# Performance work log

Hardware: AMD Instinct MI355X
Metric: run time of the kernel (lower is better)

The kernel has to match this reference:

```python
import jax, jax.numpy as jnp
import numpy as np

L, B, S, D, H = 3, 64, 512, 1024, 512  # layers, batch, seq, input(=2H), hidden


def setup_inputs() -> dict:
    key = jax.random.key(0)
    ks = jax.random.split(key, 13)
    s = lambda k, shape: jax.random.normal(k, shape, jnp.float32) * 0.02
    return {
        "x": jax.random.normal(ks[0], (B, S, D), jnp.float32),
        "fw_W": s(ks[1], (L, D + H, 3 * H)),
        "fw_b": s(ks[2], (L, 3 * H)),
        "bw_W": s(ks[3], (L, D + H, 3 * H)),
        "bw_b": s(ks[4], (L, 3 * H)),
        "h0f": s(ks[5], (L, H)),
        "c0f": s(ks[6], (L, H)),
        "h0b": s(ks[7], (L, H)),
        "c0b": s(ks[8], (L, H)),
        "proj_W": s(ks[9], (L, 2 * H, 2 * H)),
        "proj_b": s(ks[10], (L, 2 * H)),
        "in_proj_W": s(ks[11], (D, 2 * H)),
        "in_proj_b": s(ks[12], (2 * H,)),
    }


def _lstm_dir(x_tbd, W, b, h0, c0):
    """Run the coupled 3-gate cell over time. x_tbd: [S,B,D]. Returns [S,B,H]."""
    bsz = x_tbd.shape[1]

    def step(carry, xt):
        h, c = carry
        g = jnp.concatenate([xt, h], axis=-1) @ W + b  # [B, 3H]
        i, j, o = jnp.split(g, 3, axis=-1)
        i = jax.nn.sigmoid(i)
        c = (1.0 - i) * c + i * jnp.tanh(j)
        h = jnp.tanh(c) * jax.nn.sigmoid(o)
        return (h, c), h

    init = (jnp.broadcast_to(h0, (bsz, H)), jnp.broadcast_to(c0, (bsz, H)))
    _, hs = jax.lax.scan(step, init, x_tbd)
    return hs


def reference(x, fw_W, fw_b, bw_W, bw_b, h0f, c0f, h0b, c0b, proj_W, proj_b, in_proj_W, in_proj_b):
    inputs = x  # [B,S,D]
    for l in range(L):
        xt = jnp.transpose(inputs, (1, 0, 2))  # [S,B,D]
        hf = _lstm_dir(xt, fw_W[l], fw_b[l], h0f[l], c0f[l])            # [S,B,H]
        hb = _lstm_dir(xt[::-1], bw_W[l], bw_b[l], h0b[l], c0b[l])[::-1]  # [S,B,H]
        out = jnp.transpose(jnp.concatenate([hf, hb], axis=-1), (1, 0, 2))  # [B,S,2H]
        gate = jax.nn.sigmoid(out @ proj_W[l] + proj_b[l])
        if l == 0:
            inputs = x @ in_proj_W + in_proj_b  # project raw input to 2H for highway
        inputs = gate * out + (1.0 - gate) * inputs
    return inputs
```

## Files before the change

### kernel.cpp

```cpp
#include <hip/hip_runtime.h>
#include <stdint.h>

typedef short bf16x8 __attribute__((ext_vector_type(8)));
typedef short s16x4 __attribute__((ext_vector_type(4)));
typedef float f32x4 __attribute__((ext_vector_type(4)));
typedef unsigned int u32;
typedef unsigned short u16;
typedef unsigned long long u64;

#define OFF_WXT  0ull
#define OFF_WHF  18874368ull
#define OFF_CTR  28311552ull
#define OFF_PRJT 37748736ull
#define OFF_IPJT 44040192ull
#define OFF_XB   46137344ull
#define OFF_G    113246208ull
#define OFF_OCAT 314572800ull
#define OFF_INP  381681664ull
#define OFF_HB   515899392ull
#define WS_NEED  516161536ull

__device__ __forceinline__ float b2f(u32 u){ return __uint_as_float(u<<16); }
__device__ __forceinline__ u16 f2b(float f){
  u32 i = __float_as_uint(f);
  return (u16)((i + 0x7FFFu + ((i>>16)&1u))>>16);
}
__device__ __forceinline__ float sigm(float x){ return 1.f/(1.f+__expf(-x)); }
__device__ __forceinline__ float tanh_f(float x){
  x = fminf(fmaxf(x,-15.f),15.f);
  float e = __expf(2.f*x);
  return (e-1.f)/(e+1.f);
}
__device__ __forceinline__ void gl_lds16(const void* g, void* l){
  __builtin_amdgcn_global_load_lds((const __attribute__((address_space(1))) u32*)g,
                                   (__attribute__((address_space(3))) u32*)l, 16, 0, 0);
}

__global__ void k_convx(const float4* __restrict__ x, u64* __restrict__ xb){
  long i = (long)blockIdx.x*blockDim.x + threadIdx.x;
  float4 v = x[i];
  xb[i] = (u64)f2b(v.x) | ((u64)f2b(v.y)<<16) | ((u64)f2b(v.z)<<32) | ((u64)f2b(v.w)<<48);
}

__global__ __launch_bounds__(256)
void k_tr(const float* __restrict__ fw, const float* __restrict__ bw,
          const float* __restrict__ pw, const float* __restrict__ ipw,
          u16* __restrict__ wxt, u16* __restrict__ pjt, u16* __restrict__ ipjt){
  __shared__ u16 lds[64][66];
  const int b = blockIdx.x;
  const float* src; u16* dst; int srcLD, dstLD, r0, c0;
  if (b < 2304){
    int mat = b / 384, tt = b % 384;
    int kt = tt % 16, nt = tt / 16;
    int d = mat / 3, l = mat % 3;
    src = (d ? bw : fw) + (size_t)l*1536*1536; srcLD = 1536;
    dst = wxt + (size_t)mat*1536*1024;        dstLD = 1024;
    r0 = kt*64; c0 = nt*64;
  } else if (b < 3072){
    int bb = b - 2304, mat = bb / 256, tt = bb % 256;
    int kt = tt % 16, nt = tt / 16;
    src = pw + (size_t)mat*1048576; srcLD = 1024;
    dst = pjt + (size_t)mat*1048576; dstLD = 1024;
    r0 = kt*64; c0 = nt*64;
  } else {
    int tt = b - 3072;
    int kt = tt % 16, nt = tt / 16;
    src = ipw; srcLD = 1024; dst = ipjt; dstLD = 1024;
    r0 = kt*64; c0 = nt*64;
  }
  const int tr = threadIdx.x >> 6, tc = threadIdx.x & 63;
  #pragma unroll
  for (int i=0;i<16;i++){
    int r = i*4 + tr;
    lds[r][tc] = f2b(src[(size_t)(r0+r)*srcLD + c0 + tc]);
  }
  __syncthreads();
  #pragma unroll
  for (int i=0;i<16;i++){
    int nr = i*4 + tr;
    dst[(size_t)(c0+nr)*dstLD + r0 + tc] = lds[tc][nr];
  }
}

__global__ __launch_bounds__(256)
void k_whf2(const float* __restrict__ fw, const float* __restrict__ bw, u16* __restrict__ out){
  __shared__ u16 lds[64][66];
  const int b = blockIdx.x;
  const int mat = b / 192, tt = b % 192;
  const int rt = tt & 7, ct = tt >> 3;
  const int l = mat >> 1, d = mat & 1;
  const float* W = (d ? bw : fw) + (size_t)l*1536*1536;
  const int tr = threadIdx.x >> 6, tc = threadIdx.x & 63;
  #pragma unroll
  for (int i=0;i<16;i++){
    int r = i*4 + tr;
    lds[r][tc] = f2b(W[(size_t)(1024 + rt*64 + r)*1536 + ct*64 + tc]);
  }
  __syncthreads();
  const int t = threadIdx.x;
  const int lane = t >> 2;
  const int e0 = (t & 3)*2;
  u32* o32 = (u32*)out;
  #pragma unroll
  for (int kkl=0; kkl<2; ++kkl){
    int rl = kkl*32 + (lane>>4)*8 + e0;
    int kk = rt*2 + kkl;
    #pragma unroll
    for (int cg=0; cg<4; ++cg){
      int col = ct*64 + cg*16;
      int g = col >> 9;
      int wg = (col & 511) >> 4;
      size_t base16 = (size_t)l*1572864 + (size_t)((d*32+wg)*3 + g)*8192 + (size_t)kk*512;
      u16 lo = lds[rl    ][cg*16 + (lane&15)];
      u16 hi = lds[rl + 1][cg*16 + (lane&15)];
      o32[base16/2 + t] = (u32)lo | ((u32)hi<<16);
    }
  }
}

template<int V>
__global__ __launch_bounds__(256)
void gemm_bt(const u16* __restrict__ A, const u16* __restrict__ Bt,
             const float* __restrict__ bias, int K,
             u16* __restrict__ Gout, int dir,
             float* __restrict__ inputs,
             const u16* __restrict__ ocat, u16* __restrict__ xbout,
             float* __restrict__ dout)
{
  __shared__ u16 As[128*64];
  __shared__ u16 Bs[128*64];
  const int tid = threadIdx.x, wid = tid>>6, lane = tid&63;
  const int wr = wid>>1, wc = wid&1;
  const int mblk = blockIdx.x & 255;
  const int nblk = blockIdx.x >> 8;
  f32x4 acc[4][4];
  #pragma unroll
  for (int i=0;i<4;i++)
    #pragma unroll
    for (int j=0;j<4;j++) acc[i][j] = (f32x4){0.f,0.f,0.f,0.f};
  const size_t Kb = (size_t)K*2;
  const char* Ab = (const char*)A + (size_t)(mblk*128)*Kb;
  const char* Bb = (const char*)Bt + (size_t)(nblk*128)*Kb;
  const int r8 = lane>>3, c8 = lane&7;
  for (int kt=0; kt<K/64; ++kt){
    __syncthreads();
    #pragma unroll
    for (int i=0;i<4;i++){
      const int instr = wid*4 + i;
      const int row = instr*8 + r8;
      const int so = (c8*16) ^ ((row&7)<<4);
      gl_lds16(Ab + (size_t)row*Kb + kt*128 + so, (char*)As + instr*1024);
      gl_lds16(Bb + (size_t)row*Kb + kt*128 + so, (char*)Bs + instr*1024);
    }
    __syncthreads();
    #pragma unroll
    for (int ks=0; ks<2; ++ks){
      bf16x8 af[4], bfv[4];
      #pragma unroll
      for (int mt=0;mt<4;mt++){
        int r = wr*64 + mt*16 + (lane&15);
        int kb = (ks*64 + ((lane>>4)*16)) ^ ((r&7)<<4);
        af[mt] = *(const bf16x8*)((const char*)As + r*128 + kb);
      }
      #pragma unroll
      for (int nt=0;nt<4;nt++){
        int r = wc*64 + nt*16 + (lane&15);
        int kb = (ks*64 + ((lane>>4)*16)) ^ ((r&7)<<4);
        bfv[nt] = *(const bf16x8*)((const char*)Bs + r*128 + kb);
      }
      #pragma unroll
      for (int mt=0;mt<4;mt++)
        #pragma unroll
        for (int nt=0;nt<4;nt++)
          acc[mt][nt] = __builtin_amdgcn_mfma_f32_16x16x32_bf16(af[mt], bfv[nt], acc[mt][nt], 0,0,0);
    }
  }
  const int mb = mblk*128 + wr*64;
  const int nb = nblk*128 + wc*64;
  #pragma unroll
  for (int nt=0;nt<4;nt++){
    const int n = nb + nt*16 + (lane&15);
    const float bv = bias[n];
    #pragma unroll
    for (int mt=0;mt<4;mt++){
      #pragma unroll
      for (int r=0;r<4;r++){
        const int m = mb + mt*16 + (lane>>4)*4 + r;
        float v = acc[mt][nt][r] + bv;
        if (V==0){
          int b = m >> 9, t = m & 511;
          int tp = dir ? (511 - t) : t;
          int brow = b & 15;
          size_t idx = (((size_t)tp*96 + (n>>9)*32 + ((n&511)>>4))*4 + (b>>4))*256
                     + ((brow>>2)<<6) + ((n&15)<<2) + (brow&3);
          Gout[idx] = f2b(v);
        } else if (V==1){
          inputs[(size_t)m*1024 + n] = v;
        } else {
          float g = sigm(v);
          size_t a = (size_t)m*1024 + n;
          float o = b2f((u32)ocat[a]);
          float nv = g*o + (1.f-g)*inputs[a];
          if (dout) dout[a] = nv;
          else { inputs[a] = nv; xbout[a] = f2b(nv); }
        }
      }
    }
  }
}

__global__ __launch_bounds__(512, 1)
void lstm_rec(const u16* __restrict__ Whf, const u16* __restrict__ G,
              u16* __restrict__ hb,
              const float* __restrict__ h0f_, const float* __restrict__ c0f_,
              const float* __restrict__ h0b_, const float* __restrict__ c0b_,
              u16* __restrict__ ocat, u32* __restrict__ ctr, int lay)
{
  const int blk = blockIdx.x;
  const int d  = blk >> 6;
  const int bi = (blk >> 4) & 3;
  const int ci = blk & 15;
  const int tid = threadIdx.x;
  const int wave = tid >> 6, lane = tid & 63;

  __shared__ u16 hlds[16*544];
  __shared__ float ldsg[3][16][37];
  __shared__ float ldsc[16][37];

  const int g = wave >> 1, half = wave & 1;
  const bool isg = (wave < 6);

  bf16x8 w[16];
  if (isg){
    const int wgg = ci*2 + half;
    const u16* wb = Whf + (((size_t)(d*32+wgg)*3 + g)*1024 + (size_t)lane)*8;
    #pragma unroll
    for (int kk=0;kk<16;kk++) w[kk] = *(const bf16x8*)(wb + kk*512);
  }
  const float* h0 = d ? h0b_ : h0f_;
  const float* c0 = d ? c0b_ : c0f_;
  u16* hbd = hb + (size_t)d*65536;
  const u16* Gd = G + (size_t)d*50331648ull;
  u32* av = ctr + (size_t)(d*4+bi)*512;
  const u32 labase = (u32)lay * 513u;

  if (tid < 256){
    int b = tid >> 4, c2 = (tid & 15)*2;
    int col = ci*32 + c2;
    u32 pk = (u32)f2b(h0[col]) | ((u32)f2b(h0[col+1])<<16);
    __hip_atomic_store((u32*)(hbd + (size_t)(bi*16+b)*512 + col), pk,
                       __ATOMIC_RELAXED, __HIP_MEMORY_SCOPE_AGENT);
    ldsc[b][c2]   = c0[col];
    ldsc[b][c2+1] = c0[col+1];
  }
  __syncthreads();
  if (tid==0)
    __hip_atomic_store(av + ci*32, labase + 1u, __ATOMIC_RELAXED, __HIP_MEMORY_SCOPE_AGENT);

  const int ntile = g*32 + ci*2 + half;
  s16x4 q{};
  if (isg)
    q = *(const s16x4*)(Gd + (((size_t)0*96 + ntile)*4 + bi)*256 + lane*4);

  const int srow = lane >> 2;
  const int part = lane & 3;
  const int p0 = wave*2, p1 = wave*2 + 1;
  const int swzw = (srow & 7) << 4;
  char* hlrow = (char*)hlds + srow*1088;
  const int mr = lane & 15;
  const char* ab = (const char*)hlds + mr*1088;
  const int c16 = (lane>>4)*16;
  const int swzr = (mr & 7) << 4;

  for (int t=0; t<512; ++t){
    const u32 tgt = labase + (u32)t + 1u;
    const u64* hsrc = (const u64*)(hbd + (size_t)(t&1)*32768) + (size_t)bi*2048;
    while (__hip_atomic_load(av + p0*32, __ATOMIC_RELAXED, __HIP_MEMORY_SCOPE_AGENT) < tgt) {}
    while (__hip_atomic_load(av + p1*32, __ATOMIC_RELAXED, __HIP_MEMORY_SCOPE_AGENT) < tgt) {}
    asm volatile("" ::: "memory");
    u64 a0 = __hip_atomic_load(hsrc + srow*128 + p0*8 + part*2,     __ATOMIC_RELAXED, __HIP_MEMORY_SCOPE_AGENT);
    u64 a1 = __hip_atomic_load(hsrc + srow*128 + p0*8 + part*2 + 1, __ATOMIC_RELAXED, __HIP_MEMORY_SCOPE_AGENT);
    u64 b0 = __hip_atomic_load(hsrc + srow*128 + p1*8 + part*2,     __ATOMIC_RELAXED, __HIP_MEMORY_SCOPE_AGENT);
    u64 b1 = __hip_atomic_load(hsrc + srow*128 + p1*8 + part*2 + 1, __ATOMIC_RELAXED, __HIP_MEMORY_SCOPE_AGENT);
    *(u64*)(hlrow + ((p0*64 + part*16) ^ swzw))     = a0;
    *(u64*)(hlrow + ((p0*64 + part*16) ^ swzw) + 8) = a1;
    *(u64*)(hlrow + ((p1*64 + part*16) ^ swzw))     = b0;
    *(u64*)(hlrow + ((p1*64 + part*16) ^ swzw) + 8) = b1;
    __syncthreads();

    if (isg){
      f32x4 ea={0.f,0.f,0.f,0.f}, eb={0.f,0.f,0.f,0.f};
      #pragma unroll
      for (int kk=0;kk<16;kk+=2){
        bf16x8 a0v = *(const bf16x8*)(ab + ((kk*64     + c16) ^ swzr));
        bf16x8 a1v = *(const bf16x8*)(ab + ((kk*64+64  + c16) ^ swzr));
        ea = __builtin_amdgcn_mfma_f32_16x16x32_bf16(a0v, w[kk],   ea, 0,0,0);
        eb = __builtin_amdgcn_mfma_f32_16x16x32_bf16(a1v, w[kk+1], eb, 0,0,0);
      }
      const int bb = (lane>>4)*4;
      const int cc = half*16 + (lane&15);
      #pragma unroll
      for (int r=0;r<4;r++)
        ldsg[g][bb+r][cc] = ea[r] + eb[r] + b2f((u32)(u16)q[r]);
    }
    __syncthreads();

    const int t_o = d ? (511 - t) : t;
    u16* hnxt = hbd + (size_t)((t+1)&1)*32768;
    if (tid < 256){
      int b = tid>>4, c2 = (tid&15)*2;
      float i0 = sigm(ldsg[0][b][c2]);
      float i1 = sigm(ldsg[0][b][c2+1]);
      float cn0 = (1.f-i0)*ldsc[b][c2]   + i0*tanh_f(ldsg[1][b][c2]);
      float cn1 = (1.f-i1)*ldsc[b][c2+1] + i1*tanh_f(ldsg[1][b][c2+1]);
      ldsc[b][c2] = cn0; ldsc[b][c2+1] = cn1;
      float hv0 = tanh_f(cn0)*sigm(ldsg[2][b][c2]);
      float hv1 = tanh_f(cn1)*sigm(ldsg[2][b][c2+1]);
      u32 pk = (u32)f2b(hv0) | ((u32)f2b(hv1)<<16);
      int gb = bi*16 + b, col = ci*32 + c2;
      __hip_atomic_store((u32*)(hnxt + (size_t)gb*512 + col), pk,
                         __ATOMIC_RELAXED, __HIP_MEMORY_SCOPE_AGENT);
      *(u32*)(ocat + (((size_t)(gb*512 + t_o))<<10) + (d<<9) + col) = pk;
    }
    __syncthreads();

    if (tid==0)
      __hip_atomic_store(av + ci*32, labase + (u32)t + 2u,
                         __ATOMIC_RELAXED, __HIP_MEMORY_SCOPE_AGENT);
    if (isg){
      int tn = (t+1 < 512) ? (t+1) : 511;
      q = *(const s16x4*)(Gd + (((size_t)tn*96 + ntile)*4 + bi)*256 + lane*4);
    }
  }
}

extern "C" void kernel_launch(void* const* d_in, const int* in_sizes, int n_in,
                              void* d_out, int out_size, void* d_ws, size_t ws_size,
                              hipStream_t stream)
{
  (void)in_sizes; (void)n_in; (void)out_size;
  if (ws_size < WS_NEED) return;
  const float* x      = (const float*)d_in[0];
  const float* fw_W   = (const float*)d_in[1];
  const float* fw_b   = (const float*)d_in[2];
  const float* bw_W   = (const float*)d_in[3];
  const float* bw_b   = (const float*)d_in[4];
  const float* h0f    = (const float*)d_in[5];
  const float* c0f    = (const float*)d_in[6];
  const float* h0b    = (const float*)d_in[7];
  const float* c0b    = (const float*)d_in[8];
  const float* proj_W = (const float*)d_in[9];
  const float* proj_b = (const float*)d_in[10];
  const float* ipW    = (const float*)d_in[11];
  const float* ipb    = (const float*)d_in[12];
  char* ws = (char*)d_ws;
  u16* WXT  = (u16*)(ws + OFF_WXT);
  u16* WHF  = (u16*)(ws + OFF_WHF);
  u16* PRJT = (u16*)(ws + OFF_PRJT);
  u16* IPJT = (u16*)(ws + OFF_IPJT);
  u16* XB   = (u16*)(ws + OFF_XB);
  u16* GB   = (u16*)(ws + OFF_G);
  u16* OCAT = (u16*)(ws + OFF_OCAT);
  float* INP= (float*)(ws + OFF_INP);
  u16* HB   = (u16*)(ws + OFF_HB);
  u32* CTR  = (u32*)(ws + OFF_CTR);

  hipMemsetAsync(CTR, 0, 16384, stream);
  k_convx<<<32768, 256, 0, stream>>>((const float4*)x, (u64*)XB);
  k_tr<<<3328, 256, 0, stream>>>(fw_W, bw_W, proj_W, ipW, WXT, PRJT, IPJT);
  k_whf2<<<1152, 256, 0, stream>>>(fw_W, bw_W, WHF);

  gemm_bt<1><<<2048, 256, 0, stream>>>(XB, IPJT, ipb, 1024, nullptr, 0, INP, nullptr, nullptr, nullptr);

  for (int l=0; l<3; ++l){
    gemm_bt<0><<<3072, 256, 0, stream>>>(XB, WXT + (size_t)l*1572864, fw_b + l*1536, 1024,
                                         GB, 0, nullptr, nullptr, nullptr, nullptr);
    gemm_bt<0><<<3072, 256, 0, stream>>>(XB, WXT + (size_t)(3+l)*1572864, bw_b + l*1536, 1024,
                                         GB + 50331648ull, 1, nullptr, nullptr, nullptr, nullptr);
    {
      const u16* whfl = WHF + (size_t)l*1572864;
      const u16* gbp  = GB;
      u16* hbp = HB;
      const float* p1 = h0f + l*512;
      const float* p2 = c0f + l*512;
      const float* p3 = h0b + l*512;
      const float* p4 = c0b + l*512;
      u16* ocp = OCAT;
      u32* ctp = CTR;
      int lay = l;
      void* args[] = { (void*)&whfl, (void*)&gbp, (void*)&hbp,
                       (void*)&p1, (void*)&p2, (void*)&p3, (void*)&p4,
                       (void*)&ocp, (void*)&ctp, (void*)&lay };
      hipLaunchCooperativeKernel((void*)lstm_rec, dim3(128), dim3(512), args, 0, stream);
    }
    gemm_bt<2><<<2048, 256, 0, stream>>>(OCAT, PRJT + (size_t)l*1048576, proj_b + l*1024, 1024,
                                         nullptr, 0, INP, OCAT, XB,
                                         (l==2) ? (float*)d_out : nullptr);
  }
}
```

Before: 6.287 ms.

## Shrink recurrent LSTM grid to 32 blocks with all three gates per wave

Restructures the recurrent kernel so each block covers 128 hidden columns, and each wave holds the i, j and o gate weights in registers and computes all three gates for its 16 columns. The cell update then runs in registers, with no LDS round trip and one fewer barrier per step. The hidden-state output write to ocat is deferred to the next step and read from the LDS copy. This cuts the number of blocks that must synchronise across the GPU each timestep (128 to 32) and the spin-wait fanout. In exchange each block does more MFMA work per step and carries much higher register pressure from holding 48 weight vectors per lane.

```diff
diff --git a/kernel.cpp b/kernel.cpp
--- a/kernel.cpp
+++ b/kernel.cpp
@@ -209,7 +209,7 @@
   }
 }
 
-__global__ __launch_bounds__(512, 1)
+__global__ __launch_bounds__(512, 2)
 void lstm_rec(const u16* __restrict__ Whf, const u16* __restrict__ G,
               u16* __restrict__ hb,
               const float* __restrict__ h0f_, const float* __restrict__ c0f_,
@@ -217,25 +217,26 @@
               u16* __restrict__ ocat, u32* __restrict__ ctr, int lay)
 {
   const int blk = blockIdx.x;
-  const int d  = blk >> 6;
-  const int bi = (blk >> 4) & 3;
-  const int ci = blk & 15;
+  const int d  = blk >> 4;
+  const int bi = (blk >> 2) & 3;
+  const int ci = blk & 3;
   const int tid = threadIdx.x;
   const int wave = tid >> 6, lane = tid & 63;
 
   __shared__ u16 hlds[16*544];
-  __shared__ float ldsg[3][16][37];
-  __shared__ float ldsc[16][37];
-
-  const int g = wave >> 1, half = wave & 1;
-  const bool isg = (wave < 6);
-
-  bf16x8 w[16];
-  if (isg){
-    const int wgg = ci*2 + half;
-    const u16* wb = Whf + (((size_t)(d*32+wgg)*3 + g)*1024 + (size_t)lane)*8;
-    #pragma unroll
-    for (int kk=0;kk<16;kk++) w[kk] = *(const bf16x8*)(wb + kk*512);
+
+  const int nt   = ci*8 + wave;
+  const int wcol = nt*16 + (lane&15);
+
+  bf16x8 w0[16], w1[16], w2[16];
+  {
+    const u16* W = Whf + ((size_t)(d*32+nt)*3)*8192 + (size_t)lane*8;
+    #pragma unroll
+    for (int kk=0;kk<16;kk++) w0[kk] = *(const bf16x8*)(W + kk*512);
+    #pragma unroll
+    for (int kk=0;kk<16;kk++) w1[kk] = *(const bf16x8*)(W + 8192 + kk*512);
+    #pragma unroll
+    for (int kk=0;kk<16;kk++) w2[kk] = *(const bf16x8*)(W + 16384 + kk*512);
   }
   const float* h0 = d ? h0b_ : h0f_;
   const float* c0 = d ? c0b_ : c0f_;
@@ -244,92 +245,102 @@
   u32* av = ctr + (size_t)(d*4+bi)*512;
   const u32 labase = (u32)lay * 513u;
 
-  if (tid < 256){
-    int b = tid >> 4, c2 = (tid & 15)*2;
-    int col = ci*32 + c2;
+  float c[4];
+  { float cv = c0[wcol]; c[0]=cv; c[1]=cv; c[2]=cv; c[3]=cv; }
+
+  #pragma unroll
+  for (int it=0; it<2; ++it){
+    int p = tid + it*512;
+    int row = bi*16 + (p>>6);
+    int col = ci*128 + (p&63)*2;
     u32 pk = (u32)f2b(h0[col]) | ((u32)f2b(h0[col+1])<<16);
-    __hip_atomic_store((u32*)(hbd + (size_t)(bi*16+b)*512 + col), pk,
+    __hip_atomic_store((u32*)(hbd + (size_t)row*512 + col), pk,
                        __ATOMIC_RELAXED, __HIP_MEMORY_SCOPE_AGENT);
-    ldsc[b][c2]   = c0[col];
-    ldsc[b][c2+1] = c0[col+1];
   }
   __syncthreads();
   if (tid==0)
     __hip_atomic_store(av + ci*32, labase + 1u, __ATOMIC_RELAXED, __HIP_MEMORY_SCOPE_AGENT);
 
-  const int ntile = g*32 + ci*2 + half;
-  s16x4 q{};
-  if (isg)
-    q = *(const s16x4*)(Gd + (((size_t)0*96 + ntile)*4 + bi)*256 + lane*4);
-
+  s16x4 qi{}, qj{}, qo{};
+  {
+    const u16* Gt = Gd + ((size_t)nt*4 + bi)*256 + lane*4;
+    qi = *(const s16x4*)(Gt);
+    qj = *(const s16x4*)(Gt + 32768);
+    qo = *(const s16x4*)(Gt + 65536);
+  }
+
+  const int sp   = wave >> 1;
+  const int scb  = sp*128 + (wave&1)*64;
   const int srow = lane >> 2;
-  const int part = lane & 3;
-  const int p0 = wave*2, p1 = wave*2 + 1;
-  const int swzw = (srow & 7) << 4;
-  char* hlrow = (char*)hlds + srow*1088;
+  const int scol = scb + (lane&3)*16;
+  const size_t gbase = ((size_t)(bi*16+srow))*128 + (size_t)(scol>>2);
+  const int sx0  = scol*2;
+  const int swzw = (srow&7)<<4;
+  char* lrow = (char*)hlds + srow*1088;
+
   const int mr = lane & 15;
   const char* ab = (const char*)hlds + mr*1088;
   const int c16 = (lane>>4)*16;
-  const int swzr = (mr & 7) << 4;
-
-  for (int t=0; t<512; ++t){
+  const int swzr = (mr&7)<<4;
+
+  for (int t=0; t<=512; ++t){
     const u32 tgt = labase + (u32)t + 1u;
-    const u64* hsrc = (const u64*)(hbd + (size_t)(t&1)*32768) + (size_t)bi*2048;
-    while (__hip_atomic_load(av + p0*32, __ATOMIC_RELAXED, __HIP_MEMORY_SCOPE_AGENT) < tgt) {}
-    while (__hip_atomic_load(av + p1*32, __ATOMIC_RELAXED, __HIP_MEMORY_SCOPE_AGENT) < tgt) {}
+    while (__hip_atomic_load(av + sp*32, __ATOMIC_RELAXED, __HIP_MEMORY_SCOPE_AGENT) < tgt) {}
     asm volatile("" ::: "memory");
-    u64 a0 = __hip_atomic_load(hsrc + srow*128 + p0*8 + part*2,     __ATOMIC_RELAXED, __HIP_MEMORY_SCOPE_AGENT);
-    u64 a1 = __hip_atomic_load(hsrc + srow*128 + p0*8 + part*2 + 1, __ATOMIC_RELAXED, __HIP_MEMORY_SCOPE_AGENT);
-    u64 b0 = __hip_atomic_load(hsrc + srow*128 + p1*8 + part*2,     __ATOMIC_RELAXED, __HIP_MEMORY_SCOPE_AGENT);
-    u64 b1 = __hip_atomic_load(hsrc + srow*128 + p1*8 + part*2 + 1, __ATOMIC_RELAXED, __HIP_MEMORY_SCOPE_AGENT);
-    *(u64*)(hlrow + ((p0*64 + part*16) ^ swzw))     = a0;
-    *(u64*)(hlrow + ((p0*64 + part*16) ^ swzw) + 8) = a1;
-    *(u64*)(hlrow + ((p1*64 + part*16) ^ swzw))     = b0;
-    *(u64*)(hlrow + ((p1*64 + part*16) ^ swzw) + 8) = b1;
+    const u64* hsrc = (const u64*)(hbd + (size_t)(t&1)*32768);
+    u64 v0 = __hip_atomic_load(hsrc + gbase,     __ATOMIC_RELAXED, __HIP_MEMORY_SCOPE_AGENT);
+    u64 v1 = __hip_atomic_load(hsrc + gbase + 1, __ATOMIC_RELAXED, __HIP_MEMORY_SCOPE_AGENT);
+    u64 v2 = __hip_atomic_load(hsrc + gbase + 2, __ATOMIC_RELAXED, __HIP_MEMORY_SCOPE_AGENT);
+    u64 v3 = __hip_atomic_load(hsrc + gbase + 3, __ATOMIC_RELAXED, __HIP_MEMORY_SCOPE_AGENT);
+    *(u64*)(lrow + ( sx0       ^ swzw))      = v0;
+    *(u64*)(lrow + ( sx0       ^ swzw) + 8)  = v1;
+    *(u64*)(lrow + ((sx0 + 16) ^ swzw))      = v2;
+    *(u64*)(lrow + ((sx0 + 16) ^ swzw) + 8)  = v3;
     __syncthreads();
 
-    if (isg){
-      f32x4 ea={0.f,0.f,0.f,0.f}, eb={0.f,0.f,0.f,0.f};
-      #pragma unroll
-      for (int kk=0;kk<16;kk+=2){
-        bf16x8 a0v = *(const bf16x8*)(ab + ((kk*64     + c16) ^ swzr));
-        bf16x8 a1v = *(const bf16x8*)(ab + ((kk*64+64  + c16) ^ swzr));
-        ea = __builtin_amdgcn_mfma_f32_16x16x32_bf16(a0v, w[kk],   ea, 0,0,0);
-        eb = __builtin_amdgcn_mfma_f32_16x16x32_bf16(a1v, w[kk+1], eb, 0,0,0);
-      }
-      const int bb = (lane>>4)*4;
-      const int cc = half*16 + (lane&15);
-      #pragma unroll
-      for (int r=0;r<4;r++)
-        ldsg[g][bb+r][cc] = ea[r] + eb[r] + b2f((u32)(u16)q[r]);
-    }
-    __syncthreads();
-
-    const int t_o = d ? (511 - t) : t;
+    if (t > 0){
+      int lr = ci*4 + (tid>>7);
+      int col4 = (tid&127)*4;
+      u64 hv = *(const u64*)((const char*)hlds + lr*1088 + ((col4*2) ^ ((lr&7)<<4)));
+      int t_o = d ? (512 - t) : (t - 1);
+      *(u64*)(ocat + (size_t)((bi*16+lr)*512 + t_o)*1024 + (d<<9) + col4) = hv;
+    }
+    if (t == 512) break;
+
+    f32x4 ai={0.f,0.f,0.f,0.f}, aj={0.f,0.f,0.f,0.f}, ao={0.f,0.f,0.f,0.f};
+    #pragma unroll
+    for (int kk=0;kk<16;kk++){
+      bf16x8 a = *(const bf16x8*)(ab + ((kk*64 + c16) ^ swzr));
+      ai = __builtin_amdgcn_mfma_f32_16x16x32_bf16(a, w0[kk], ai, 0,0,0);
+      aj = __builtin_amdgcn_mfma_f32_16x16x32_bf16(a, w1[kk], aj, 0,0,0);
+      ao = __builtin_amdgcn_mfma_f32_16x16x32_bf16(a, w2[kk], ao, 0,0,0);
+    }
+
     u16* hnxt = hbd + (size_t)((t+1)&1)*32768;
-    if (tid < 256){
-      int b = tid>>4, c2 = (tid&15)*2;
-      float i0 = sigm(ldsg[0][b][c2]);
-      float i1 = sigm(ldsg[0][b][c2+1]);
-      float cn0 = (1.f-i0)*ldsc[b][c2]   + i0*tanh_f(ldsg[1][b][c2]);
-      float cn1 = (1.f-i1)*ldsc[b][c2+1] + i1*tanh_f(ldsg[1][b][c2+1]);
-      ldsc[b][c2] = cn0; ldsc[b][c2+1] = cn1;
-      float hv0 = tanh_f(cn0)*sigm(ldsg[2][b][c2]);
-      float hv1 = tanh_f(cn1)*sigm(ldsg[2][b][c2+1]);
-      u32 pk = (u32)f2b(hv0) | ((u32)f2b(hv1)<<16);
-      int gb = bi*16 + b, col = ci*32 + c2;
-      __hip_atomic_store((u32*)(hnxt + (size_t)gb*512 + col), pk,
+    #pragma unroll
+    for (int r=0;r<4;r++){
+      float gi = sigm(ai[r] + b2f((u32)(u16)qi[r]));
+      float gj = tanh_f(aj[r] + b2f((u32)(u16)qj[r]));
+      float go = sigm(ao[r] + b2f((u32)(u16)qo[r]));
+      float cn = (1.f-gi)*c[r] + gi*gj;
+      c[r] = cn;
+      u16 hvb = f2b(tanh_f(cn)*go);
+      int row = bi*16 + (lane>>4)*4 + r;
+      __hip_atomic_store(hnxt + (size_t)row*512 + wcol, hvb,
                          __ATOMIC_RELAXED, __HIP_MEMORY_SCOPE_AGENT);
-      *(u32*)(ocat + (((size_t)(gb*512 + t_o))<<10) + (d<<9) + col) = pk;
     }
     __syncthreads();
 
     if (tid==0)
       __hip_atomic_store(av + ci*32, labase + (u32)t + 2u,
                          __ATOMIC_RELAXED, __HIP_MEMORY_SCOPE_AGENT);
-    if (isg){
+
+    {
       int tn = (t+1 < 512) ? (t+1) : 511;
-      q = *(const s16x4*)(Gd + (((size_t)tn*96 + ntile)*4 + bi)*256 + lane*4);
+      const u16* Gt = Gd + ((size_t)(tn*96 + nt)*4 + bi)*256 + lane*4;
+      qi = *(const s16x4*)(Gt);
+      qj = *(const s16x4*)(Gt + 32768);
+      qo = *(const s16x4*)(Gt + 65536);
     }
   }
 }
@@ -391,7 +402,7 @@
       void* args[] = { (void*)&whfl, (void*)&gbp, (void*)&hbp,
                        (void*)&p1, (void*)&p2, (void*)&p3, (void*)&p4,
                        (void*)&ocp, (void*)&ctp, (void*)&lay };
-      hipLaunchCooperativeKernel((void*)lstm_rec, dim3(128), dim3(512), args, 0, stream);
+      hipLaunchCooperativeKernel((void*)lstm_rec, dim3(32), dim3(512), args, 0, stream);
     }
     gemm_bt<2><<<2048, 256, 0, stream>>>(OCAT, PRJT + (size_t)l*1048576, proj_b + l*1024, 1024,
                                          nullptr, 0, INP, OCAT, XB,
```

After: 8.101 ms. 1.29x slower.

## Load recurrent h directly into MFMA registers, dropping the LDS stage and barrier

Applied to the files above, without the earlier changes.

Each gate wave now polls all 16 producer flags with a wave-wide vote, then loads its MFMA A-operand rows of h straight from global memory into registers. This removes the cooperative copy of h into LDS and one __syncthreads per timestep, which shortens the serial per-step critical path. In exchange every gate wave issues redundant global loads of the same h tile (six waves read the same data) and spins on the flags itself, which raises L2 traffic and register pressure.

```diff
diff --git a/kernel.cpp b/kernel.cpp
--- a/kernel.cpp
+++ b/kernel.cpp
@@ -223,7 +223,6 @@
   const int tid = threadIdx.x;
   const int wave = tid >> 6, lane = tid & 63;
 
-  __shared__ u16 hlds[16*544];
   __shared__ float ldsg[3][16][37];
   __shared__ float ldsc[16][37];
 
@@ -262,40 +261,33 @@
   if (isg)
     q = *(const s16x4*)(Gd + (((size_t)0*96 + ntile)*4 + bi)*256 + lane*4);
 
-  const int srow = lane >> 2;
-  const int part = lane & 3;
-  const int p0 = wave*2, p1 = wave*2 + 1;
-  const int swzw = (srow & 7) << 4;
-  char* hlrow = (char*)hlds + srow*1088;
-  const int mr = lane & 15;
-  const char* ab = (const char*)hlds + mr*1088;
-  const int c16 = (lane>>4)*16;
-  const int swzr = (mr & 7) << 4;
+  const int arow = bi*16 + (lane&15);
+  const int koff = (lane>>4)*16;
+  const u32* fp = av + (lane&15)*32;
 
   for (int t=0; t<512; ++t){
     const u32 tgt = labase + (u32)t + 1u;
-    const u64* hsrc = (const u64*)(hbd + (size_t)(t&1)*32768) + (size_t)bi*2048;
-    while (__hip_atomic_load(av + p0*32, __ATOMIC_RELAXED, __HIP_MEMORY_SCOPE_AGENT) < tgt) {}
-    while (__hip_atomic_load(av + p1*32, __ATOMIC_RELAXED, __HIP_MEMORY_SCOPE_AGENT) < tgt) {}
-    asm volatile("" ::: "memory");
-    u64 a0 = __hip_atomic_load(hsrc + srow*128 + p0*8 + part*2,     __ATOMIC_RELAXED, __HIP_MEMORY_SCOPE_AGENT);
-    u64 a1 = __hip_atomic_load(hsrc + srow*128 + p0*8 + part*2 + 1, __ATOMIC_RELAXED, __HIP_MEMORY_SCOPE_AGENT);
-    u64 b0 = __hip_atomic_load(hsrc + srow*128 + p1*8 + part*2,     __ATOMIC_RELAXED, __HIP_MEMORY_SCOPE_AGENT);
-    u64 b1 = __hip_atomic_load(hsrc + srow*128 + p1*8 + part*2 + 1, __ATOMIC_RELAXED, __HIP_MEMORY_SCOPE_AGENT);
-    *(u64*)(hlrow + ((p0*64 + part*16) ^ swzw))     = a0;
-    *(u64*)(hlrow + ((p0*64 + part*16) ^ swzw) + 8) = a1;
-    *(u64*)(hlrow + ((p1*64 + part*16) ^ swzw))     = b0;
-    *(u64*)(hlrow + ((p1*64 + part*16) ^ swzw) + 8) = b1;
-    __syncthreads();
-
     if (isg){
+      for (;;){
+        u32 fl = __hip_atomic_load(fp, __ATOMIC_RELAXED, __HIP_MEMORY_SCOPE_AGENT);
+        if (__all((int)(fl >= tgt))) break;
+      }
+      asm volatile("" ::: "memory");
+      const char* hrow = (const char*)hbd + (size_t)(t&1)*65536
+                       + (size_t)arow*1024 + koff;
+      bf16x8 a[16];
+      #pragma unroll
+      for (int kk=0;kk<16;kk++){
+        union { u64 q2[2]; bf16x8 v; } u;
+        u.q2[0] = __hip_atomic_load((const u64*)(hrow + kk*64),     __ATOMIC_RELAXED, __HIP_MEMORY_SCOPE_AGENT);
+        u.q2[1] = __hip_atomic_load((const u64*)(hrow + kk*64 + 8), __ATOMIC_RELAXED, __HIP_MEMORY_SCOPE_AGENT);
+        a[kk] = u.v;
+      }
       f32x4 ea={0.f,0.f,0.f,0.f}, eb={0.f,0.f,0.f,0.f};
       #pragma unroll
       for (int kk=0;kk<16;kk+=2){
-        bf16x8 a0v = *(const bf16x8*)(ab + ((kk*64     + c16) ^ swzr));
-        bf16x8 a1v = *(const bf16x8*)(ab + ((kk*64+64  + c16) ^ swzr));
-        ea = __builtin_amdgcn_mfma_f32_16x16x32_bf16(a0v, w[kk],   ea, 0,0,0);
-        eb = __builtin_amdgcn_mfma_f32_16x16x32_bf16(a1v, w[kk+1], eb, 0,0,0);
+        ea = __builtin_amdgcn_mfma_f32_16x16x32_bf16(a[kk],   w[kk],   ea, 0,0,0);
+        eb = __builtin_amdgcn_mfma_f32_16x16x32_bf16(a[kk+1], w[kk+1], eb, 0,0,0);
       }
       const int bb = (lane>>4)*4;
       const int cc = half*16 + (lane&15);
```

Result: slower. 12.62 ms (+100.7%).

## Split per-block step flags into per-wave flags with finer-grained readiness

Applied to the files above, without the earlier changes.

Each recurrent block now publishes four per-wave progress counters instead of a single one. Each elementwise wave stores its slice of h, waits on its own memory counter, and then bumps its flag without waiting for a block barrier. Consumers spin only on the flag covering the 8-column slice they actually load. This shortens the critical path of the cross-block handoff at each timestep, at the cost of more flag polling traffic and a remapped thread-to-element layout in the cell update.

```diff
diff --git a/kernel.cpp b/kernel.cpp
--- a/kernel.cpp
+++ b/kernel.cpp
@@ -241,7 +241,7 @@
   const float* c0 = d ? c0b_ : c0f_;
   u16* hbd = hb + (size_t)d*65536;
   const u16* Gd = G + (size_t)d*50331648ull;
-  u32* av = ctr + (size_t)(d*4+bi)*512;
+  u32* av = ctr + (size_t)(d*4+bi)*2048;
   const u32 labase = (u32)lay * 513u;
 
   if (tid < 256){
@@ -254,8 +254,9 @@
     ldsc[b][c2+1] = c0[col+1];
   }
   __syncthreads();
-  if (tid==0)
-    __hip_atomic_store(av + ci*32, labase + 1u, __ATOMIC_RELAXED, __HIP_MEMORY_SCOPE_AGENT);
+  if (tid < 4)
+    __hip_atomic_store(av + (ci*4 + tid)*32, labase + 1u,
+                       __ATOMIC_RELAXED, __HIP_MEMORY_SCOPE_AGENT);
 
   const int ntile = g*32 + ci*2 + half;
   s16x4 q{};
@@ -265,6 +266,8 @@
   const int srow = lane >> 2;
   const int part = lane & 3;
   const int p0 = wave*2, p1 = wave*2 + 1;
+  const u32* f0 = av + (p0*4 + part)*32;
+  const u32* f1 = av + (p1*4 + part)*32;
   const int swzw = (srow & 7) << 4;
   char* hlrow = (char*)hlds + srow*1088;
   const int mr = lane & 15;
@@ -275,8 +278,8 @@
   for (int t=0; t<512; ++t){
     const u32 tgt = labase + (u32)t + 1u;
     const u64* hsrc = (const u64*)(hbd + (size_t)(t&1)*32768) + (size_t)bi*2048;
-    while (__hip_atomic_load(av + p0*32, __ATOMIC_RELAXED, __HIP_MEMORY_SCOPE_AGENT) < tgt) {}
-    while (__hip_atomic_load(av + p1*32, __ATOMIC_RELAXED, __HIP_MEMORY_SCOPE_AGENT) < tgt) {}
+    while (__hip_atomic_load(f0, __ATOMIC_RELAXED, __HIP_MEMORY_SCOPE_AGENT) < tgt) {}
+    while (__hip_atomic_load(f1, __ATOMIC_RELAXED, __HIP_MEMORY_SCOPE_AGENT) < tgt) {}
     asm volatile("" ::: "memory");
     u64 a0 = __hip_atomic_load(hsrc + srow*128 + p0*8 + part*2,     __ATOMIC_RELAXED, __HIP_MEMORY_SCOPE_AGENT);
     u64 a1 = __hip_atomic_load(hsrc + srow*128 + p0*8 + part*2 + 1, __ATOMIC_RELAXED, __HIP_MEMORY_SCOPE_AGENT);
@@ -308,25 +311,28 @@
     const int t_o = d ? (511 - t) : t;
     u16* hnxt = hbd + (size_t)((t+1)&1)*32768;
     if (tid < 256){
-      int b = tid>>4, c2 = (tid&15)*2;
-      float i0 = sigm(ldsg[0][b][c2]);
-      float i1 = sigm(ldsg[0][b][c2+1]);
-      float cn0 = (1.f-i0)*ldsc[b][c2]   + i0*tanh_f(ldsg[1][b][c2]);
-      float cn1 = (1.f-i1)*ldsc[b][c2+1] + i1*tanh_f(ldsg[1][b][c2+1]);
-      ldsc[b][c2] = cn0; ldsc[b][c2+1] = cn1;
-      float hv0 = tanh_f(cn0)*sigm(ldsg[2][b][c2]);
-      float hv1 = tanh_f(cn1)*sigm(ldsg[2][b][c2+1]);
+      int wv = tid >> 6;
+      int r  = (tid >> 2) & 15;
+      int c2 = wv*8 + (tid & 3)*2;
+      float i0 = sigm(ldsg[0][r][c2]);
+      float i1 = sigm(ldsg[0][r][c2+1]);
+      float cn0 = (1.f-i0)*ldsc[r][c2]   + i0*tanh_f(ldsg[1][r][c2]);
+      float cn1 = (1.f-i1)*ldsc[r][c2+1] + i1*tanh_f(ldsg[1][r][c2+1]);
+      ldsc[r][c2] = cn0; ldsc[r][c2+1] = cn1;
+      float hv0 = tanh_f(cn0)*sigm(ldsg[2][r][c2]);
+      float hv1 = tanh_f(cn1)*sigm(ldsg[2][r][c2+1]);
       u32 pk = (u32)f2b(hv0) | ((u32)f2b(hv1)<<16);
-      int gb = bi*16 + b, col = ci*32 + c2;
+      int gb = bi*16 + r, col = ci*32 + c2;
       __hip_atomic_store((u32*)(hnxt + (size_t)gb*512 + col), pk,
                          __ATOMIC_RELAXED, __HIP_MEMORY_SCOPE_AGENT);
       *(u32*)(ocat + (((size_t)(gb*512 + t_o))<<10) + (d<<9) + col) = pk;
+      asm volatile("s_waitcnt vmcnt(0)" ::: "memory");
+      if ((tid & 63) == 0)
+        __hip_atomic_store(av + (ci*4 + wv)*32, labase + (u32)t + 2u,
+                           __ATOMIC_RELAXED, __HIP_MEMORY_SCOPE_AGENT);
     }
     __syncthreads();
 
-    if (tid==0)
-      __hip_atomic_store(av + ci*32, labase + (u32)t + 2u,
-                         __ATOMIC_RELAXED, __HIP_MEMORY_SCOPE_AGENT);
     if (isg){
       int tn = (t+1 < 512) ? (t+1) : 511;
       q = *(const s16x4*)(Gd + (((size_t)tn*96 + ntile)*4 + bi)*256 + lane*4);
@@ -365,7 +371,7 @@
   u16* HB   = (u16*)(ws + OFF_HB);
   u32* CTR  = (u32*)(ws + OFF_CTR);
 
-  hipMemsetAsync(CTR, 0, 16384, stream);
+  hipMemsetAsync(CTR, 0, 65536, stream);
   k_convx<<<32768, 256, 0, stream>>>((const float4*)x, (u64*)XB);
   k_tr<<<3328, 256, 0, stream>>>(fw_W, bw_W, proj_W, ipW, WXT, PRJT, IPJT);
   k_whf2<<<1152, 256, 0, stream>>>(fw_W, bw_W, WHF);
```

Result: slower. 7.153 ms (+13.8%).
